# Kernel tuning notes

Hardware: AMD Instinct MI355X
Metric: run time of the kernel (lower is better)

Reference implementation:

```python
import jax, jax.numpy as jnp
import numpy as np

NUM_TOKENS = 131072
N_EXPERTS = 256
N_GROUP = 8
TOPK_GROUP = 4
TOP_K = 8
ROUTED_SCALING = 2.5


def setup_inputs() -> dict:
    key = jax.random.key(0)
    k1, k2 = jax.random.split(key)
    router_logits = jax.random.normal(k1, (NUM_TOKENS, N_EXPERTS), dtype=jnp.float32)
    correction_bias = jax.random.normal(k2, (N_EXPERTS,), dtype=jnp.float32) * 0.1
    return {"router_logits": router_logits, "correction_bias": correction_bias}


def reference(router_logits, correction_bias):
    T = router_logits.shape[0]
    eg = N_EXPERTS // N_GROUP  # experts per group = 32

    scores = jax.nn.sigmoid(router_logits).astype(jnp.float32)          # [T, 256]
    scores_for_choice = scores + correction_bias[None, :]                # [T, 256]

    # group score = sum of top-2 corrected scores within each group
    grp = scores_for_choice.reshape(T, N_GROUP, eg)                      # [T, 8, 32]
    top2, _ = jax.lax.top_k(grp, 2)                                      # [T, 8, 2]
    group_scores = top2.sum(axis=-1)                                     # [T, 8]

    # pick top groups, build expert-level mask
    _, group_idx = jax.lax.top_k(group_scores, TOPK_GROUP)               # [T, 4]
    rows = jnp.arange(T)[:, None]
    group_mask = jnp.zeros_like(group_scores).at[rows, group_idx].set(1.0)  # [T, 8]
    score_mask = jnp.repeat(group_mask, eg, axis=-1)                     # [T, 256]

    masked_scores = jnp.where(score_mask > 0, scores_for_choice, 0.0)
    _, topk_indices = jax.lax.top_k(masked_scores, TOP_K)                # [T, 8]

    topk_weights = jnp.take_along_axis(scores, topk_indices, axis=1)     # [T, 8]
    denom = topk_weights.sum(axis=-1, keepdims=True) + 1e-20
    topk_weights = topk_weights / denom * ROUTED_SCALING
    return (topk_indices, topk_weights)
```

## Files before the change

### kernel.cpp

```cpp
#include <hip/hip_runtime.h>
#include <math.h>


constexpr int N_EXPERTS  = 256;
constexpr int N_GROUP    = 8;
constexpr int EG         = 32;
constexpr int TOPK_GROUP = 4;
constexpr int TOP_K      = 8;
constexpr int BLOCK      = 512;
constexpr int TPB_TOK    = BLOCK / N_GROUP;

typedef unsigned int u32;
typedef unsigned long long u64;

__device__ __forceinline__ u32 fmono(float f) {
  const u32 u = __float_as_uint(f);
  return u ^ ((u32)((int)u >> 31) | 0x80000000u);
}
__device__ __forceinline__ float fmono_inv(u32 m) {
  const u32 u = (m & 0x80000000u) ? (m ^ 0x80000000u) : ~m;
  return __uint_as_float(u);
}
__device__ __forceinline__ u64 mkkey(float v, int idx) {
  return ((u64)fmono(v) << 32) | (u32)(255 - idx);
}
__device__ __forceinline__ int key_idx(u64 k) { return 255 - (int)(k & 0xFFu); }
__device__ __forceinline__ float key_val(u64 k) { return fmono_inv((u32)(k >> 32)); }

__device__ __forceinline__ float recip_nr(float d) {
  float r = __builtin_amdgcn_rcpf(d);
  r = __builtin_fmaf(__builtin_fmaf(-d, r, 1.0f), r, r);
  r = __builtin_fmaf(__builtin_fmaf(-d, r, 1.0f), r, r);
  return r;
}

__device__ __forceinline__ void kswap(u64& a, u64& b) {
  const bool sw = b > a;
  const u64 t = sw ? b : a;
  b = sw ? a : b;
  a = t;
}

__device__ __forceinline__ void sort8(u64 (&k)[8]) {
  kswap(k[0], k[1]); kswap(k[2], k[3]); kswap(k[4], k[5]); kswap(k[6], k[7]);
  kswap(k[0], k[2]); kswap(k[1], k[3]); kswap(k[4], k[6]); kswap(k[5], k[7]);
  kswap(k[1], k[2]); kswap(k[5], k[6]);
  kswap(k[0], k[4]); kswap(k[1], k[5]); kswap(k[2], k[6]); kswap(k[3], k[7]);
  kswap(k[2], k[4]); kswap(k[3], k[5]);
  kswap(k[1], k[2]); kswap(k[3], k[4]); kswap(k[5], k[6]);
}

__device__ __forceinline__ void merge8(u64 (&A)[8], const u64 (&B)[8]) {
  u64 R[8];
#pragma unroll
  for (int i = 0; i < 8; ++i) {
    const bool a = A[i] >= B[7 - i];
    R[i] = a ? A[i] : B[7 - i];
  }
  kswap(R[0], R[4]); kswap(R[1], R[5]); kswap(R[2], R[6]); kswap(R[3], R[7]);
  kswap(R[0], R[2]); kswap(R[1], R[3]); kswap(R[4], R[6]); kswap(R[5], R[7]);
  kswap(R[0], R[1]); kswap(R[2], R[3]); kswap(R[4], R[5]); kswap(R[6], R[7]);
#pragma unroll
  for (int i = 0; i < 8; ++i) A[i] = R[i];
}

__device__ __forceinline__ void load_list(const ulonglong2 (*kb)[4], int j,
                                          int s, u64 (&L)[8]) {
  const int r  = 8 * j + s;
  const int rr = r ^ ((j >> 2) & 1);
  const int sw = j & 3;
#pragma unroll
  for (int p = 0; p < 4; ++p) {
    const ulonglong2 v = kb[rr][p ^ sw];
    L[2 * p]     = v.x;
    L[2 * p + 1] = v.y;
  }
}

__global__ __launch_bounds__(BLOCK, 4) void deepseek_topk_router_r10(
    const float* __restrict__ logits,
    const float* __restrict__ bias,
    float* __restrict__ out,
    int T) {
  __shared__ __align__(16) float gsb[BLOCK];
  __shared__ ulonglong2 kbuf[BLOCK][4];

  const int tid = threadIdx.x;
  const int id  = blockIdx.x * BLOCK + tid;
  const int t   = id >> 3;
  const int q   = id & 7;

  const float4* row4 =
      reinterpret_cast<const float4*>(logits + (size_t)t * N_EXPERTS + q * EG);
  const float4* b4 = reinterpret_cast<const float4*>(bias + q * EG);

  float4 x[8];
#pragma unroll
  for (int u = 0; u < 8; ++u) x[u] = row4[u];
  float4 bb[8];
#pragma unroll
  for (int u = 0; u < 8; ++u) bb[u] = b4[u];

  u64 K[8];
#pragma unroll
  for (int c = 0; c < 4; ++c) {
    u64 C[8];
    const float xs[8] = {x[2*c].x, x[2*c].y, x[2*c].z, x[2*c].w,
                         x[2*c+1].x, x[2*c+1].y, x[2*c+1].z, x[2*c+1].w};
    const float bs[8] = {bb[2*c].x, bb[2*c].y, bb[2*c].z, bb[2*c].w,
                         bb[2*c+1].x, bb[2*c+1].y, bb[2*c+1].z, bb[2*c+1].w};
#pragma unroll
    for (int j = 0; j < 8; ++j) {
      const float e = expf(-xs[j]);
      const float s = recip_nr(1.0f + e);
      C[j] = mkkey(s + bs[j], q * EG + c * 8 + j);
    }
    sort8(C);
    if (c == 0) {
#pragma unroll
      for (int j = 0; j < 8; ++j) K[j] = C[j];
    } else {
      merge8(K, C);
    }
  }

  gsb[tid] = key_val(K[0]) + key_val(K[1]);
  {
    const int rr = tid ^ ((tid >> 5) & 1);
    const int sw = (tid >> 3) & 3;
    kbuf[rr][0 ^ sw] = make_ulonglong2(K[0], K[1]);
    kbuf[rr][1 ^ sw] = make_ulonglong2(K[2], K[3]);
    kbuf[rr][2 ^ sw] = make_ulonglong2(K[4], K[5]);
    kbuf[rr][3 ^ sw] = make_ulonglong2(K[6], K[7]);
  }
  __syncthreads();
  if (tid >= TPB_TOK) return;

  const int j   = tid;
  const int tok = blockIdx.x * TPB_TOK + j;

  const float4* gp = reinterpret_cast<const float4*>(&gsb[8 * j]);
  const float4 ga = gp[0], gb = gp[1];
  const float g[N_GROUP] = {ga.x, ga.y, ga.z, ga.w, gb.x, gb.y, gb.z, gb.w};

  int s0 = 0, s1 = 0, s2 = 0, s3 = 0, cnt = 0;
#pragma unroll
  for (int h = 0; h < N_GROUP; ++h) {
    int rank = 0;
#pragma unroll
    for (int m = 0; m < N_GROUP; ++m)
      rank += (m < h) ? (g[m] >= g[h] ? 1 : 0) : (g[m] > g[h] ? 1 : 0);
    const bool pick = (rank < TOPK_GROUP);
    s0 = (pick && cnt == 0) ? h : s0;
    s1 = (pick && cnt == 1) ? h : s1;
    s2 = (pick && cnt == 2) ? h : s2;
    s3 = (pick && cnt == 3) ? h : s3;
    cnt += pick ? 1 : 0;
  }

  u64 A[8], B[8];
  load_list(kbuf, j, s0, A);
  load_list(kbuf, j, s1, B);
  merge8(A, B);
  load_list(kbuf, j, s2, B);
  merge8(A, B);
  load_list(kbuf, j, s3, B);
  merge8(A, B);

  float fi[8], sv[8];
  float sum = 0.0f;
#pragma unroll
  for (int k = 0; k < TOP_K; ++k) {
    const int idx = key_idx(A[k]);
    const float c = key_val(A[k]);
    sv[k] = c - bias[idx];
    fi[k] = (float)idx;
    sum += sv[k];
  }
  const float scale = 2.5f / (sum + 1e-20f);

  float4* oi = reinterpret_cast<float4*>(out) + (size_t)tok * 2;
  oi[0] = make_float4(fi[0], fi[1], fi[2], fi[3]);
  oi[1] = make_float4(fi[4], fi[5], fi[6], fi[7]);
  float4* ow = reinterpret_cast<float4*>(out + (size_t)T * TOP_K) + (size_t)tok * 2;
  ow[0] = make_float4(sv[0] * scale, sv[1] * scale, sv[2] * scale, sv[3] * scale);
  ow[1] = make_float4(sv[4] * scale, sv[5] * scale, sv[6] * scale, sv[7] * scale);
}

extern "C" void kernel_launch(void* const* d_in, const int* in_sizes, int n_in,
                              void* d_out, int out_size, void* d_ws, size_t ws_size,
                              hipStream_t stream) {
  const float* logits = (const float*)d_in[0];
  const float* bias   = (const float*)d_in[1];
  float* out = (float*)d_out;
  const int T = in_sizes[0] / N_EXPERTS;
  const int blocks = T / TPB_TOK;
  deepseek_topk_router_r10<<<blocks, BLOCK, 0, stream>>>(logits, bias, out, T);
}
```

Baseline: 207.7 us.

## Make router kernel persistent with register prefetch and rotating phase-B warps

Converts the one-slice-per-block kernel into a persistent kernel with a fixed grid of 512 blocks, each looping over several 64-token slices. The next slice's logits are prefetched into registers while the current chunks are sorted. The per-token final merge is rotated across wavefronts so the same wave does not always do the serial tail. Bias is staged once in LDS for both the score correction and the final lookup. This is meant to hide global load latency and reduce launch and tail imbalance. It costs an extra barrier per iteration and gives less parallelism per launch.

```diff
diff --git a/kernel.cpp b/kernel.cpp
--- a/kernel.cpp
+++ b/kernel.cpp
@@ -69,6 +69,7 @@
   const int r  = 8 * j + s;
   const int rr = r ^ ((j >> 2) & 1);
   const int sw = j & 3;
+  (void)r;
 #pragma unroll
   for (int p = 0; p < 4; ++p) {
     const ulonglong2 v = kb[rr][p ^ sw];
@@ -77,68 +78,47 @@
   }
 }
 
-__global__ __launch_bounds__(BLOCK, 4) void deepseek_topk_router_r10(
-    const float* __restrict__ logits,
-    const float* __restrict__ bias,
-    float* __restrict__ out,
-    int T) {
-  __shared__ __align__(16) float gsb[BLOCK];
-  __shared__ ulonglong2 kbuf[BLOCK][4];
-
-  const int tid = threadIdx.x;
-  const int id  = blockIdx.x * BLOCK + tid;
-  const int t   = id >> 3;
-  const int q   = id & 7;
-
-  const float4* row4 =
-      reinterpret_cast<const float4*>(logits + (size_t)t * N_EXPERTS + q * EG);
-  const float4* b4 = reinterpret_cast<const float4*>(bias + q * EG);
-
-  float4 x[8];
-#pragma unroll
-  for (int u = 0; u < 8; ++u) x[u] = row4[u];
-  float4 bb[8];
-#pragma unroll
-  for (int u = 0; u < 8; ++u) bb[u] = b4[u];
-
-  u64 K[8];
-#pragma unroll
-  for (int c = 0; c < 4; ++c) {
-    u64 C[8];
-    const float xs[8] = {x[2*c].x, x[2*c].y, x[2*c].z, x[2*c].w,
-                         x[2*c+1].x, x[2*c+1].y, x[2*c+1].z, x[2*c+1].w};
-    const float bs[8] = {bb[2*c].x, bb[2*c].y, bb[2*c].z, bb[2*c].w,
-                         bb[2*c+1].x, bb[2*c+1].y, bb[2*c+1].z, bb[2*c+1].w};
-#pragma unroll
-    for (int j = 0; j < 8; ++j) {
-      const float e = expf(-xs[j]);
-      const float s = recip_nr(1.0f + e);
-      C[j] = mkkey(s + bs[j], q * EG + c * 8 + j);
-    }
-    sort8(C);
-    if (c == 0) {
-#pragma unroll
-      for (int j = 0; j < 8; ++j) K[j] = C[j];
-    } else {
-      merge8(K, C);
-    }
-  }
-
-  gsb[tid] = key_val(K[0]) + key_val(K[1]);
-  {
-    const int rr = tid ^ ((tid >> 5) & 1);
-    const int sw = (tid >> 3) & 3;
-    kbuf[rr][0 ^ sw] = make_ulonglong2(K[0], K[1]);
-    kbuf[rr][1 ^ sw] = make_ulonglong2(K[2], K[3]);
-    kbuf[rr][2 ^ sw] = make_ulonglong2(K[4], K[5]);
-    kbuf[rr][3 ^ sw] = make_ulonglong2(K[6], K[7]);
-  }
-  __syncthreads();
-  if (tid >= TPB_TOK) return;
-
-  const int j   = tid;
-  const int tok = blockIdx.x * TPB_TOK + j;
-
+__device__ __forceinline__ void chunk_sort(u64 (&K)[8], const float4 xa,
+                                           const float4 xb, const float4 ba,
+                                           const float4 bv, const int idx0,
+                                           const bool first) {
+  u64 C[8];
+  const float xs[8] = {xa.x, xa.y, xa.z, xa.w, xb.x, xb.y, xb.z, xb.w};
+  const float bs[8] = {ba.x, ba.y, ba.z, ba.w, bv.x, bv.y, bv.z, bv.w};
+#pragma unroll
+  for (int j = 0; j < 8; ++j) {
+    const float e = expf(-xs[j]);
+    const float s = recip_nr(1.0f + e);
+    C[j] = mkkey(s + bs[j], idx0 + j);
+  }
+  sort8(C);
+  if (first) {
+#pragma unroll
+    for (int j = 0; j < 8; ++j) K[j] = C[j];
+  } else {
+    merge8(K, C);
+  }
+}
+
+__device__ __forceinline__ void phase_a(u64 (&K)[8], float4 (&x)[8],
+                                        const float4* brow, const float4*& rp,
+                                        const int qbase, const bool pf) {
+  chunk_sort(K, x[0], x[1], brow[0], brow[1], qbase + 0,  true);
+  chunk_sort(K, x[2], x[3], brow[2], brow[3], qbase + 8,  false);
+  if (pf) { x[0] = rp[0]; x[1] = rp[1]; x[2] = rp[2]; x[3] = rp[3]; }
+  chunk_sort(K, x[4], x[5], brow[4], brow[5], qbase + 16, false);
+  chunk_sort(K, x[6], x[7], brow[6], brow[7], qbase + 24, false);
+  if (pf) {
+    x[4] = rp[4]; x[5] = rp[5]; x[6] = rp[6]; x[7] = rp[7];
+    rp += (TPB_TOK * N_EXPERTS) / 4;
+  }
+}
+
+__device__ __forceinline__ void phase_b(const float* gsb,
+                                        const ulonglong2 (*kbuf)[4],
+                                        const float (*bias_lds)[36],
+                                        float* out, const int T,
+                                        const int j, const int tok) {
   const float4* gp = reinterpret_cast<const float4*>(&gsb[8 * j]);
   const float4 ga = gp[0], gb = gp[1];
   const float g[N_GROUP] = {ga.x, ga.y, ga.z, ga.w, gb.x, gb.y, gb.z, gb.w};
@@ -158,14 +138,11 @@
     cnt += pick ? 1 : 0;
   }
 
-  u64 A[8], B[8];
+  u64 A[8], Bv[8];
   load_list(kbuf, j, s0, A);
-  load_list(kbuf, j, s1, B);
-  merge8(A, B);
-  load_list(kbuf, j, s2, B);
-  merge8(A, B);
-  load_list(kbuf, j, s3, B);
-  merge8(A, B);
+  load_list(kbuf, j, s1, Bv); merge8(A, Bv);
+  load_list(kbuf, j, s2, Bv); merge8(A, Bv);
+  load_list(kbuf, j, s3, Bv); merge8(A, Bv);
 
   float fi[8], sv[8];
   float sum = 0.0f;
@@ -173,7 +150,7 @@
   for (int k = 0; k < TOP_K; ++k) {
     const int idx = key_idx(A[k]);
     const float c = key_val(A[k]);
-    sv[k] = c - bias[idx];
+    sv[k] = c - bias_lds[idx >> 5][idx & 31];
     fi[k] = (float)idx;
     sum += sv[k];
   }
@@ -185,6 +162,61 @@
   float4* ow = reinterpret_cast<float4*>(out + (size_t)T * TOP_K) + (size_t)tok * 2;
   ow[0] = make_float4(sv[0] * scale, sv[1] * scale, sv[2] * scale, sv[3] * scale);
   ow[1] = make_float4(sv[4] * scale, sv[5] * scale, sv[6] * scale, sv[7] * scale);
+}
+
+__global__ __launch_bounds__(BLOCK, 4) void deepseek_topk_router_r11(
+    const float* __restrict__ logits,
+    const float* __restrict__ bias,
+    float* __restrict__ out,
+    int T) {
+  __shared__ __align__(16) float gsb[BLOCK];
+  __shared__ ulonglong2 kbuf[BLOCK][4];
+  __shared__ __align__(16) float bias_lds[N_GROUP][36];
+
+  const int tid = threadIdx.x;
+  const int lq  = tid & 7;
+  const int lt  = tid >> 3;
+  const int nIter  = (T / TPB_TOK) / gridDim.x;
+  const int slice0 = blockIdx.x * nIter;
+  const int qbase  = lq * EG;
+
+  if (tid < N_EXPERTS) bias_lds[tid >> 5][tid & 31] = bias[tid];
+
+  const float4* rp = reinterpret_cast<const float4*>(
+      logits + ((size_t)(slice0 * TPB_TOK + lt)) * N_EXPERTS + qbase);
+  float4 x[8];
+#pragma unroll
+  for (int u = 0; u < 8; ++u) x[u] = rp[u];
+  rp += (TPB_TOK * N_EXPERTS) / 4;
+
+  __syncthreads();
+
+  const float4* brow = reinterpret_cast<const float4*>(bias_lds[lq]);
+
+  u64 K[8];
+  phase_a(K, x, brow, rp, qbase, nIter > 1);
+
+  for (int i = 0; i < nIter; ++i) {
+    gsb[tid] = key_val(K[0]) + key_val(K[1]);
+    {
+      const int rr = tid ^ ((tid >> 5) & 1);
+      const int sw = (tid >> 3) & 3;
+      kbuf[rr][0 ^ sw] = make_ulonglong2(K[0], K[1]);
+      kbuf[rr][1 ^ sw] = make_ulonglong2(K[2], K[3]);
+      kbuf[rr][2 ^ sw] = make_ulonglong2(K[4], K[5]);
+      kbuf[rr][3 ^ sw] = make_ulonglong2(K[6], K[7]);
+    }
+    __syncthreads();
+
+    if ((tid >> 6) == (i & 7))
+      phase_b(gsb, kbuf, bias_lds, out, T, tid & 63,
+              (slice0 + i) * TPB_TOK + (tid & 63));
+
+    if (i + 1 < nIter) {
+      phase_a(K, x, brow, rp, qbase, i + 2 < nIter);
+      __syncthreads();
+    }
+  }
 }
 
 extern "C" void kernel_launch(void* const* d_in, const int* in_sizes, int n_in,
@@ -194,6 +226,8 @@
   const float* bias   = (const float*)d_in[1];
   float* out = (float*)d_out;
   const int T = in_sizes[0] / N_EXPERTS;
-  const int blocks = T / TPB_TOK;
-  deepseek_topk_router_r10<<<blocks, BLOCK, 0, stream>>>(logits, bias, out, T);
-}
+  const int nSlices = T / TPB_TOK;
+  int grid = 512;
+  if (nSlices % grid != 0) grid = nSlices;
+  deepseek_topk_router_r11<<<grid, BLOCK, 0, stream>>>(logits, bias, out, T);
+}
```

After: 232.2 us. 11.8% more time.
